# Performance work log

Hardware: AMD Instinct MI355X
Metric: run time of the kernel (lower is better)

Reference implementation:

```python
import jax, jax.numpy as jnp
import numpy as np

NEG_SLOPE = 0.2  # PyG GATConv default leaky_relu slope


def gat_layer(x, src, dst, W, a_src, a_dst, bias, heads, d, concat):
    # x: [N, in_dim]; src/dst: [E] (edges flow src -> dst, self-loops included)
    N = x.shape[0]
    h = (x @ W).reshape(N, heads, d)                      # [N, H, D]
    alpha_src = jnp.einsum('nhd,hd->nh', h, a_src)        # [N, H]
    alpha_dst = jnp.einsum('nhd,hd->nh', h, a_dst)        # [N, H]
    e = jax.nn.leaky_relu(alpha_src[src] + alpha_dst[dst], NEG_SLOPE)  # [E, H]
    # softmax over incoming edges of each destination node (segment softmax)
    m = jax.ops.segment_max(e, dst, num_segments=N)       # [N, H]
    ex = jnp.exp(e - m[dst])
    s = jax.ops.segment_sum(ex, dst, num_segments=N)      # [N, H]
    alpha = ex / s[dst]                                   # [E, H]
    msg = h[src] * alpha[..., None]                       # [E, H, D]
    out = jax.ops.segment_sum(msg, dst, num_segments=N)   # [N, H, D]
    out = out.reshape(N, heads * d) if concat else out.mean(axis=1)
    return out + bias


def setup_inputs() -> dict:
    key = jax.random.key(0)
    ks = jax.random.split(key, 12)
    N, E = 10000, 320000
    in_dim, hidden, heads, out_dim = 256, 64, 4, 40
    x = jax.random.normal(ks[0], (N, in_dim), dtype=jnp.float32)
    edge_index = jax.random.randint(ks[1], (2, E), 0, N, dtype=jnp.int64)
    s = 0.1
    return {
        'x': x,
        'edge_index': edge_index,
        'W1': jax.random.normal(ks[2], (in_dim, heads * hidden), jnp.float32) * s,
        'att_src1': jax.random.normal(ks[3], (heads, hidden), jnp.float32) * s,
        'att_dst1': jax.random.normal(ks[4], (heads, hidden), jnp.float32) * s,
        'bias1': jnp.zeros((heads * hidden,), jnp.float32),
        'W2': jax.random.normal(ks[5], (heads * hidden, out_dim), jnp.float32) * s,
        'att_src2': jax.random.normal(ks[6], (1, out_dim), jnp.float32) * s,
        'att_dst2': jax.random.normal(ks[7], (1, out_dim), jnp.float32) * s,
        'bias2': jnp.zeros((out_dim,), jnp.float32),
    }


def reference(x, edge_index, W1, att_src1, att_dst1, bias1, W2, att_src2, att_dst2, bias2):
    N = x.shape[0]
    # PyG GATConv adds self-loops by default
    loop = jnp.arange(N, dtype=edge_index.dtype)
    src = jnp.concatenate([edge_index[0], loop])
    dst = jnp.concatenate([edge_index[1], loop])
    h = gat_layer(x, src, dst, W1, att_src1, att_dst1, bias1, heads=4, d=64, concat=True)
    h = jax.nn.relu(h)
    out = gat_layer(h, src, dst, W2, att_src2, att_dst2, bias2, heads=1, d=40, concat=False)
    return jax.nn.log_softmax(out, axis=1)
```

## Files before the change

### kernel.cpp

```cpp
#include <hip/hip_runtime.h>
#include <hip/hip_bf16.h>
#include <math.h>

#define IN_DIM 256
#define C1 256
#define H1 4
#define OUT_DIM 40
#define W2PAD 48
#define NEG_SLOPE 0.2f
#define DSTRIDE 128

typedef __attribute__((ext_vector_type(8))) short bf16x8;
typedef __attribute__((ext_vector_type(4))) float f32x4;
typedef __attribute__((ext_vector_type(2))) float f32x2;

#define XS_LD 264

__device__ __forceinline__ unsigned short f2bf(float f) {
    union { float f; unsigned u; } c; c.f = f;
    unsigned r = c.u + 0x7fffu + ((c.u >> 16) & 1u);
    return (unsigned short)(r >> 16);
}

__device__ __forceinline__ unsigned char f2fp8(float f) {
    return (unsigned char)__builtin_amdgcn_cvt_pk_fp8_f32(f, 0.f, 0, false);
}

__device__ __forceinline__ float sel4(float4 v, int h) {
    float r = v.x;
    r = (h == 1) ? v.y : r;
    r = (h == 2) ? v.z : r;
    r = (h == 3) ? v.w : r;
    return r;
}

__device__ __forceinline__ float leaky(float v) {
    return (v >= 0.0f) ? v : NEG_SLOPE * v;
}

__global__ void k_prep(int* __restrict__ fill, const float* __restrict__ W1,
                       unsigned short* __restrict__ W1t, const float* __restrict__ W2,
                       unsigned short* __restrict__ W2t, const float* __restrict__ a_src2,
                       const float* __restrict__ a_dst2, float* __restrict__ w2s,
                       float* __restrict__ w2d, int N) {
    int t = threadIdx.x;
    int g = blockIdx.x * 256 + t;
    if (g < N) fill[g << 4] = 0;
    if (g < C1) {
        float s = 0.0f, d = 0.0f;
#pragma unroll
        for (int j = 0; j < OUT_DIM; ++j) {
            float w = W2[g * OUT_DIM + j];
            s += w * a_src2[j];
            d += w * a_dst2[j];
        }
        w2s[g] = s;
        w2d[g] = d;
    }
    if (g < W2PAD * C1) {
        int j = g >> 8, k = g & 255;
        W2t[g] = (j < OUT_DIM) ? f2bf(W2[k * OUT_DIM + j]) : 0;
    }
    __shared__ float s32[32][33];
    int b = blockIdx.x;
    int r0 = (b >> 3) * 32;
    int c0 = (b & 7) * 32;
    for (int i = t; i < 1024; i += 256) {
        int lr = i >> 5, lc = i & 31;
        s32[lr][lc] = W1[(r0 + lr) * 256 + c0 + lc];
    }
    __syncthreads();
    for (int i = t; i < 1024; i += 256) {
        int oc = i >> 5, ok = i & 31;
        W1t[(c0 + oc) * 256 + r0 + ok] = f2bf(s32[ok][oc]);
    }
}

__global__ void __launch_bounds__(256) k_fused1(
    const float* __restrict__ x, const unsigned short* __restrict__ W1t,
    const float* __restrict__ a_src, const float* __restrict__ a_dst,
    unsigned char* __restrict__ h1, float* __restrict__ as1, float* __restrict__ ad1,
    const int* __restrict__ ei, int* __restrict__ fill, unsigned short* __restrict__ srcs,
    int N, int E, int ET, int G1) {
    __shared__ unsigned short xs[64 * XS_LD];
    int t = threadIdx.x;

    if (blockIdx.x >= G1) {
        int eb = (blockIdx.x - G1) * 1024 + t;
#pragma unroll
        for (int k = 0; k < 4; ++k) {
            int e = eb + k * 256;
            if (e < ET) {
                int s, d;
                if (e < E) { s = ei[e]; d = ei[E + e]; }
                else       { s = e - E; d = s; }
                int pos = atomicAdd(&fill[d << 4], 1);
                srcs[(d << 7) + pos] = (unsigned short)s;
            }
        }
        return;
    }

    int n0 = blockIdx.x * 64;
    for (int i = t; i < 4096; i += 256) {
        int r = i >> 6, c4 = i & 63;
        int n = n0 + r;
        float4 v = (n < N) ? ((const float4*)x)[(size_t)n * 64 + c4]
                           : make_float4(0.f, 0.f, 0.f, 0.f);
        uint2 pk;
        pk.x = (unsigned)f2bf(v.x) | ((unsigned)f2bf(v.y) << 16);
        pk.y = (unsigned)f2bf(v.z) | ((unsigned)f2bf(v.w) << 16);
        *((uint2*)&xs[r * XS_LD + c4 * 4]) = pk;
    }
    __syncthreads();

    int wv = t >> 6, lane = t & 63;
    int quad = lane >> 4, ln = lane & 15;

    f32x4 acc[4][4];
#pragma unroll
    for (int mt = 0; mt < 4; ++mt)
#pragma unroll
        for (int nt = 0; nt < 4; ++nt) acc[mt][nt] = (f32x4){0.f, 0.f, 0.f, 0.f};

#pragma unroll
    for (int kb = 0; kb < 8; ++kb) {
        bf16x8 af[4], bf[4];
#pragma unroll
        for (int mt = 0; mt < 4; ++mt)
            af[mt] = *((bf16x8*)&xs[(mt * 16 + ln) * XS_LD + kb * 32 + quad * 8]);
#pragma unroll
        for (int nt = 0; nt < 4; ++nt)
            bf[nt] = *((const bf16x8*)(W1t + ((wv * 64 + nt * 16 + ln) * 256 + kb * 32 + quad * 8)));
#pragma unroll
        for (int mt = 0; mt < 4; ++mt)
#pragma unroll
            for (int nt = 0; nt < 4; ++nt)
                acc[mt][nt] = __builtin_amdgcn_mfma_f32_16x16x32_bf16(af[mt], bf[nt], acc[mt][nt], 0, 0, 0);
    }

    float asv[4], adv[4];
#pragma unroll
    for (int nt = 0; nt < 4; ++nt) {
        int col = wv * 64 + nt * 16 + ln;
        asv[nt] = a_src[col];
        adv[nt] = a_dst[col];
    }
#pragma unroll
    for (int mt = 0; mt < 4; ++mt) {
        float ds[4] = {0.f, 0.f, 0.f, 0.f};
        float dd[4] = {0.f, 0.f, 0.f, 0.f};
#pragma unroll
        for (int nt = 0; nt < 4; ++nt) {
#pragma unroll
            for (int r = 0; r < 4; ++r) {
                float v = acc[mt][nt][r];
                ds[r] += v * asv[nt];
                dd[r] += v * adv[nt];
            }
        }
#pragma unroll
        for (int r = 0; r < 4; ++r) {
            float vs = ds[r], vd = dd[r];
#pragma unroll
            for (int o = 1; o < 16; o <<= 1) {
                vs += __shfl_xor(vs, o);
                vd += __shfl_xor(vd, o);
            }
            if (ln == 0) {
                int node = n0 + mt * 16 + quad * 4 + r;
                if (node < N) {
                    as1[node * H1 + wv] = vs;
                    ad1[node * H1 + wv] = vd;
                }
            }
        }
    }

    __syncthreads();
    unsigned char* bt = (unsigned char*)xs;
#pragma unroll
    for (int mt = 0; mt < 4; ++mt)
#pragma unroll
        for (int nt = 0; nt < 4; ++nt)
#pragma unroll
            for (int r = 0; r < 4; ++r)
                bt[(mt * 16 + quad * 4 + r) * 256 + wv * 64 + nt * 16 + ln] = f2fp8(acc[mt][nt][r]);
    __syncthreads();
    const uint4* bt4 = (const uint4*)bt;
    uint4* h14 = (uint4*)(h1 + (size_t)n0 * C1);
    for (int i = t; i < 1024; i += 256) {
        int row = i >> 4;
        if (n0 + row < N) h14[i] = bt4[i];
    }
}

__global__ void __launch_bounds__(256) k_node1(
    const int* __restrict__ fill, const unsigned short* __restrict__ srcs,
    const float* __restrict__ as1f, const float* __restrict__ ad1f,
    const unsigned char* __restrict__ h1, const float* __restrict__ bias1,
    const float* __restrict__ w2s, const float* __restrict__ w2d,
    unsigned short* __restrict__ agg1b, float* __restrict__ as2,
    float* __restrict__ ad2, int N) {
    int w = threadIdx.x >> 6, lane = threadIdx.x & 63;
    int n = blockIdx.x * 4 + w;
    if (n >= N) return;
    __shared__ float4 es[4][64];
    int start = n << 7;
    int end = start + fill[n << 4];
    const float4* as4 = (const float4*)as1f;
    float4 adn = ((const float4*)ad1f)[n];
    int h = lane >> 4;
    const float* esw = (const float*)&es[w][0];

    float4 S4 = make_float4(0.f, 0.f, 0.f, 0.f);
    float ac0 = 0.f, ac1 = 0.f, ac2 = 0.f, ac3 = 0.f;

    for (int c = start; c < end; c += 64) {
        int cnt = min(64, end - c);
        int idx = c + lane;
        int sreg = (idx < end) ? (int)srcs[idx] : 0;
        float4 ex = make_float4(0.f, 0.f, 0.f, 0.f);
        if (idx < end) {
            float4 a = as4[sreg];
            ex.x = __expf(leaky(a.x + adn.x));
            ex.y = __expf(leaky(a.y + adn.y));
            ex.z = __expf(leaky(a.z + adn.z));
            ex.w = __expf(leaky(a.w + adn.w));
        }
        S4.x += ex.x; S4.y += ex.y; S4.z += ex.z; S4.w += ex.w;
        es[w][lane] = ex;

        int i = 0;
        for (; i + 7 < cnt; i += 8) {
            int s[8]; float a[8]; unsigned r[8];
#pragma unroll
            for (int k = 0; k < 8; ++k) {
                s[k] = __shfl(sreg, i + k);
                a[k] = esw[(i + k) * 4 + h];
            }
#pragma unroll
            for (int k = 0; k < 8; ++k)
                r[k] = ((const unsigned*)(h1 + (size_t)s[k] * C1))[lane];
#pragma unroll
            for (int k = 0; k < 8; ++k) {
                f32x2 lo = __builtin_amdgcn_cvt_pk_f32_fp8(r[k], false);
                f32x2 hi = __builtin_amdgcn_cvt_pk_f32_fp8(r[k], true);
                ac0 += a[k] * lo.x;
                ac1 += a[k] * lo.y;
                ac2 += a[k] * hi.x;
                ac3 += a[k] * hi.y;
            }
        }
        for (; i < cnt; ++i) {
            int s0 = __shfl(sreg, i);
            float a0 = esw[i * 4 + h];
            unsigned r0 = ((const unsigned*)(h1 + (size_t)s0 * C1))[lane];
            f32x2 lo = __builtin_amdgcn_cvt_pk_f32_fp8(r0, false);
            f32x2 hi = __builtin_amdgcn_cvt_pk_f32_fp8(r0, true);
            ac0 += a0 * lo.x;
            ac1 += a0 * lo.y;
            ac2 += a0 * hi.x;
            ac3 += a0 * hi.y;
        }
    }

#pragma unroll
    for (int o = 32; o > 0; o >>= 1) {
        S4.x += __shfl_xor(S4.x, o);
        S4.y += __shfl_xor(S4.y, o);
        S4.z += __shfl_xor(S4.z, o);
        S4.w += __shfl_xor(S4.w, o);
    }
    float iS = 1.0f / sel4(S4, h);
    float4 b = ((const float4*)bias1)[lane];
    float v0 = fmaxf(ac0 * iS + b.x, 0.f);
    float v1 = fmaxf(ac1 * iS + b.y, 0.f);
    float v2 = fmaxf(ac2 * iS + b.z, 0.f);
    float v3 = fmaxf(ac3 * iS + b.w, 0.f);
    uint2 pk;
    pk.x = (unsigned)f2bf(v0) | ((unsigned)f2bf(v1) << 16);
    pk.y = (unsigned)f2bf(v2) | ((unsigned)f2bf(v3) << 16);
    ((uint2*)(agg1b + (size_t)n * C1))[lane] = pk;

    float4 ws = ((const float4*)w2s)[lane];
    float4 wd = ((const float4*)w2d)[lane];
    float ps = v0 * ws.x + v1 * ws.y + v2 * ws.z + v3 * ws.w;
    float pd = v0 * wd.x + v1 * wd.y + v2 * wd.z + v3 * wd.w;
#pragma unroll
    for (int o = 32; o > 0; o >>= 1) {
        ps += __shfl_xor(ps, o);
        pd += __shfl_xor(pd, o);
    }
    if (lane == 0) { as2[n] = ps; ad2[n] = pd; }
}

__global__ void __launch_bounds__(256) k_gemm2m(
    const unsigned short* __restrict__ agg1b, const unsigned short* __restrict__ W2t,
    unsigned short* __restrict__ h2b, int N) {
    int t = threadIdx.x;
    int wv = t >> 6, lane = t & 63;
    int quad = lane >> 4, ln = lane & 15;
    int n0 = blockIdx.x * 64;
    int mrow = n0 + wv * 16 + ln;

    f32x4 acc[3];
#pragma unroll
    for (int nt = 0; nt < 3; ++nt) acc[nt] = (f32x4){0.f, 0.f, 0.f, 0.f};

#pragma unroll
    for (int kb = 0; kb < 8; ++kb) {
        bf16x8 af = *((const bf16x8*)(agg1b + (size_t)mrow * C1 + kb * 32 + quad * 8));
#pragma unroll
        for (int nt = 0; nt < 3; ++nt) {
            bf16x8 bfr = *((const bf16x8*)(W2t + ((nt * 16 + ln) * C1 + kb * 32 + quad * 8)));
            acc[nt] = __builtin_amdgcn_mfma_f32_16x16x32_bf16(af, bfr, acc[nt], 0, 0, 0);
        }
    }
#pragma unroll
    for (int nt = 0; nt < 3; ++nt) {
        int col = nt * 16 + ln;
        if (col < OUT_DIM) {
#pragma unroll
            for (int r = 0; r < 4; ++r) {
                int node = n0 + wv * 16 + quad * 4 + r;
                if (node < N) h2b[(size_t)node * OUT_DIM + col] = f2bf(acc[nt][r]);
            }
        }
    }
}

__global__ void __launch_bounds__(256) k_node2(
    const int* __restrict__ fill, const unsigned short* __restrict__ srcs,
    const float* __restrict__ as2, const float* __restrict__ ad2,
    const unsigned short* __restrict__ h2b, const float* __restrict__ bias2,
    float* __restrict__ out, int N) {
    int w = threadIdx.x >> 6, lane = threadIdx.x & 63;
    int n = blockIdx.x * 4 + w;
    if (n >= N) return;
    int start = n << 7;
    int end = start + fill[n << 4];
    float adn = ad2[n];
    float S = 0.f, acc0 = 0.f, acc1 = 0.f;
    bool act = lane < 20;

    for (int c = start; c < end; c += 64) {
        int cnt = min(64, end - c);
        int idx = c + lane;
        int sreg = (idx < end) ? (int)srcs[idx] : 0;
        float ex = (idx < end) ? __expf(leaky(as2[sreg] + adn)) : 0.f;
        S += ex;
        int i = 0;
        for (; i + 3 < cnt; i += 4) {
            int su[4]; float al[4]; unsigned rw[4];
#pragma unroll
            for (int k = 0; k < 4; ++k) {
                su[k] = __shfl(sreg, i + k);
                al[k] = __shfl(ex, i + k);
            }
#pragma unroll
            for (int k = 0; k < 4; ++k)
                rw[k] = act ? *(const unsigned*)(h2b + (size_t)su[k] * OUT_DIM + lane * 2) : 0u;
#pragma unroll
            for (int k = 0; k < 4; ++k) {
                acc0 += al[k] * __uint_as_float(rw[k] << 16);
                acc1 += al[k] * __uint_as_float(rw[k] & 0xffff0000u);
            }
        }
        for (; i < cnt; ++i) {
            int su0 = __shfl(sreg, i);
            float al0 = __shfl(ex, i);
            unsigned rw0 = act ? *(const unsigned*)(h2b + (size_t)su0 * OUT_DIM + lane * 2) : 0u;
            acc0 += al0 * __uint_as_float(rw0 << 16);
            acc1 += al0 * __uint_as_float(rw0 & 0xffff0000u);
        }
    }
#pragma unroll
    for (int o = 32; o > 0; o >>= 1) S += __shfl_xor(S, o);

    float v0 = act ? (acc0 / S + bias2[lane * 2]) : -INFINITY;
    float v1 = act ? (acc1 / S + bias2[lane * 2 + 1]) : -INFINITY;
    float mx = fmaxf(v0, v1);
#pragma unroll
    for (int o = 16; o > 0; o >>= 1) mx = fmaxf(mx, __shfl_xor(mx, o));
    float e0 = act ? __expf(v0 - mx) : 0.f;
    float e1 = act ? __expf(v1 - mx) : 0.f;
    float esum = e0 + e1;
#pragma unroll
    for (int o = 16; o > 0; o >>= 1) esum += __shfl_xor(esum, o);
    if (act) {
        float l = mx + logf(esum);
        out[(size_t)n * OUT_DIM + lane * 2]     = v0 - l;
        out[(size_t)n * OUT_DIM + lane * 2 + 1] = v1 - l;
    }
}

extern "C" void kernel_launch(void* const* d_in, const int* in_sizes, int n_in,
                              void* d_out, int out_size, void* d_ws, size_t ws_size,
                              hipStream_t stream) {
    const float* x        = (const float*)d_in[0];
    const int*   ei       = (const int*)d_in[1];
    const float* W1       = (const float*)d_in[2];
    const float* att_src1 = (const float*)d_in[3];
    const float* att_dst1 = (const float*)d_in[4];
    const float* bias1    = (const float*)d_in[5];
    const float* W2       = (const float*)d_in[6];
    const float* att_src2 = (const float*)d_in[7];
    const float* att_dst2 = (const float*)d_in[8];
    const float* bias2    = (const float*)d_in[9];
    float* out = (float*)d_out;

    const int N  = in_sizes[0] / IN_DIM;
    const int E  = in_sizes[1] / 2;
    const int ET = E + N;
    const int Npad = (N + 63) & ~63;

    char* base = (char*)d_ws;
    auto alloc = [&](size_t bytes) {
        char* p = base;
        base += (bytes + 255) & ~(size_t)255;
        return p;
    };
    unsigned char*  h1    = (unsigned char*)alloc((size_t)N * C1);
    unsigned short* W1t   = (unsigned short*)alloc((size_t)C1 * C1 * 2);
    unsigned short* W2t   = (unsigned short*)alloc((size_t)W2PAD * C1 * 2);
    unsigned short* agg1b = (unsigned short*)alloc((size_t)Npad * C1 * 2);
    unsigned short* h2b   = (unsigned short*)alloc((size_t)N * OUT_DIM * 2);
    float* as1   = (float*)alloc((size_t)N * H1 * 4);
    float* ad1   = (float*)alloc((size_t)N * H1 * 4);
    float* as2   = (float*)alloc((size_t)N * 4);
    float* ad2   = (float*)alloc((size_t)N * 4);
    float* w2s   = (float*)alloc((size_t)C1 * 4);
    float* w2d   = (float*)alloc((size_t)C1 * 4);
    int* fill    = (int*)alloc((size_t)N * 16 * 4);
    unsigned short* srcs = (unsigned short*)alloc((size_t)N * DSTRIDE * 2);

    const int G1 = (N + 63) / 64;
    const int GS = (ET + 1023) / 1024;

    k_prep<<<64, 256, 0, stream>>>(fill, W1, W1t, W2, W2t, att_src2, att_dst2, w2s, w2d, N);
    k_fused1<<<G1 + GS, 256, 0, stream>>>(x, W1t, att_src1, att_dst1, h1, as1, ad1,
                                          ei, fill, srcs, N, E, ET, G1);
    k_node1<<<(N + 3) / 4, 256, 0, stream>>>(fill, srcs, as1, ad1, h1, bias1, w2s, w2d,
                                             agg1b, as2, ad2, N);
    k_gemm2m<<<(N + 63) / 64, 256, 0, stream>>>(agg1b, W2t, h2b, N);
    k_node2<<<(N + 3) / 4, 256, 0, stream>>>(fill, srcs, as2, ad2, h2b, bias2, out, N);
}
```

Measured before the change: 142.6 us.

## Shard per-destination edge counters to cut atomic contention in CSR build

Replaces the single per-destination fill counter with eight sharded counters, chosen by edge index, each with its own slot region in a wider per-node source list. This spreads atomicAdd traffic on hot destination counters across separate cache lines. The cost is a larger fill array to zero and read, a prefix sum over eight shard counts per node, and a per-lane shard lookup when gathering sources in both aggregation kernels. Each shard holds at most 24 slots, so a destination that receives more than 24 edges in one shard would overflow its slots.

```diff
diff --git a/kernel.cpp b/kernel.cpp
--- a/kernel.cpp
+++ b/kernel.cpp
@@ -8,7 +8,9 @@
 #define OUT_DIM 40
 #define W2PAD 48
 #define NEG_SLOPE 0.2f
-#define DSTRIDE 128
+#define NSHARD 8
+#define SHSLOT 24
+#define DSTRIDE 192
 
 typedef __attribute__((ext_vector_type(8))) short bf16x8;
 typedef __attribute__((ext_vector_type(4))) float f32x4;
@@ -45,7 +47,7 @@
                        float* __restrict__ w2d, int N) {
     int t = threadIdx.x;
     int g = blockIdx.x * 256 + t;
-    if (g < N) fill[g << 4] = 0;
+    for (int i = g; i < N * NSHARD; i += 64 * 256) fill[i << 4] = 0;
     if (g < C1) {
         float s = 0.0f, d = 0.0f;
 #pragma unroll
@@ -94,8 +96,9 @@
                 int s, d;
                 if (e < E) { s = ei[e]; d = ei[E + e]; }
                 else       { s = e - E; d = s; }
-                int pos = atomicAdd(&fill[d << 4], 1);
-                srcs[(d << 7) + pos] = (unsigned short)s;
+                int j = e & (NSHARD - 1);
+                int pos = atomicAdd(&fill[((d << 3) + j) << 4], 1);
+                srcs[d * DSTRIDE + j * SHSLOT + pos] = (unsigned short)s;
             }
         }
         return;
@@ -206,8 +209,13 @@
     int n = blockIdx.x * 4 + w;
     if (n >= N) return;
     __shared__ float4 es[4][64];
-    int start = n << 7;
-    int end = start + fill[n << 4];
+    int off[NSHARD + 1];
+    off[0] = 0;
+#pragma unroll
+    for (int j = 0; j < NSHARD; ++j)
+        off[j + 1] = off[j] + fill[((n << 3) + j) << 4];
+    int deg = off[NSHARD];
+    const unsigned short* srow = srcs + (size_t)n * DSTRIDE;
     const float4* as4 = (const float4*)as1f;
     float4 adn = ((const float4*)ad1f)[n];
     int h = lane >> 4;
@@ -216,12 +224,19 @@
     float4 S4 = make_float4(0.f, 0.f, 0.f, 0.f);
     float ac0 = 0.f, ac1 = 0.f, ac2 = 0.f, ac3 = 0.f;
 
-    for (int c = start; c < end; c += 64) {
-        int cnt = min(64, end - c);
+    for (int c = 0; c < deg; c += 64) {
+        int cnt = min(64, deg - c);
         int idx = c + lane;
-        int sreg = (idx < end) ? (int)srcs[idx] : 0;
+        int sreg = 0;
+        if (idx < deg) {
+            int jj = 0, bo = 0;
+#pragma unroll
+            for (int j = 1; j < NSHARD; ++j)
+                if (idx >= off[j]) { jj = j; bo = off[j]; }
+            sreg = (int)srow[jj * SHSLOT + (idx - bo)];
+        }
         float4 ex = make_float4(0.f, 0.f, 0.f, 0.f);
-        if (idx < end) {
+        if (idx < deg) {
             float4 a = as4[sreg];
             ex.x = __expf(leaky(a.x + adn.x));
             ex.y = __expf(leaky(a.y + adn.y));
@@ -338,17 +353,29 @@
     int w = threadIdx.x >> 6, lane = threadIdx.x & 63;
     int n = blockIdx.x * 4 + w;
     if (n >= N) return;
-    int start = n << 7;
-    int end = start + fill[n << 4];
+    int off[NSHARD + 1];
+    off[0] = 0;
+#pragma unroll
+    for (int j = 0; j < NSHARD; ++j)
+        off[j + 1] = off[j] + fill[((n << 3) + j) << 4];
+    int deg = off[NSHARD];
+    const unsigned short* srow = srcs + (size_t)n * DSTRIDE;
     float adn = ad2[n];
     float S = 0.f, acc0 = 0.f, acc1 = 0.f;
     bool act = lane < 20;
 
-    for (int c = start; c < end; c += 64) {
-        int cnt = min(64, end - c);
+    for (int c = 0; c < deg; c += 64) {
+        int cnt = min(64, deg - c);
         int idx = c + lane;
-        int sreg = (idx < end) ? (int)srcs[idx] : 0;
-        float ex = (idx < end) ? __expf(leaky(as2[sreg] + adn)) : 0.f;
+        int sreg = 0;
+        if (idx < deg) {
+            int jj = 0, bo = 0;
+#pragma unroll
+            for (int j = 1; j < NSHARD; ++j)
+                if (idx >= off[j]) { jj = j; bo = off[j]; }
+            sreg = (int)srow[jj * SHSLOT + (idx - bo)];
+        }
+        float ex = (idx < deg) ? __expf(leaky(as2[sreg] + adn)) : 0.f;
         S += ex;
         int i = 0;
         for (; i + 3 < cnt; i += 4) {
@@ -432,7 +459,7 @@
     float* ad2   = (float*)alloc((size_t)N * 4);
     float* w2s   = (float*)alloc((size_t)C1 * 4);
     float* w2d   = (float*)alloc((size_t)C1 * 4);
-    int* fill    = (int*)alloc((size_t)N * 16 * 4);
+    int* fill    = (int*)alloc((size_t)N * NSHARD * 16 * 4);
     unsigned short* srcs = (unsigned short*)alloc((size_t)N * DSTRIDE * 2);
 
     const int G1 = (N + 63) / 64;
```

New measurement: 145.0 us. No clear change (+1.7%).

## Split each node's edge aggregation across two waves in layer-1 node kernel

Applied to the files above, without the earlier changes.

The layer-1 node kernel now assigns two wavefronts per destination node, each handling alternating edges, instead of one wavefront per node. Each wave stages its own exp weights. Partial softmax sums and accumulators are combined through shared memory after a block barrier. The goal is more parallelism and more memory-latency hiding for the per-node fp8 row gathers. The trade-off is twice as many waves, extra barriers, and a single-pass design that relies on degree never exceeding 128. Separately, the edge-scatter blocks in the fused GEMM kernel now process 8 edges per thread instead of 4, halving the number of scatter blocks.

```diff
diff --git a/kernel.cpp b/kernel.cpp
--- a/kernel.cpp
+++ b/kernel.cpp
@@ -86,9 +86,9 @@
     int t = threadIdx.x;
 
     if (blockIdx.x >= G1) {
-        int eb = (blockIdx.x - G1) * 1024 + t;
-#pragma unroll
-        for (int k = 0; k < 4; ++k) {
+        int eb = (blockIdx.x - G1) * 2048 + t;
+#pragma unroll
+        for (int k = 0; k < 8; ++k) {
             int e = eb + k * 256;
             if (e < ET) {
                 int s, d;
@@ -202,69 +202,36 @@
     const float* __restrict__ w2s, const float* __restrict__ w2d,
     unsigned short* __restrict__ agg1b, float* __restrict__ as2,
     float* __restrict__ ad2, int N) {
-    int w = threadIdx.x >> 6, lane = threadIdx.x & 63;
-    int n = blockIdx.x * 4 + w;
-    if (n >= N) return;
+    int wv = threadIdx.x >> 6, lane = threadIdx.x & 63;
+    int nl = wv >> 1;
+    int half = wv & 1;
+    int n = blockIdx.x * 2 + nl;
     __shared__ float4 es[4][64];
-    int start = n << 7;
-    int end = start + fill[n << 4];
+    __shared__ float4 sS[4];
+    __shared__ float4 accb[2][64];
+    bool valid = (n < N);
+
+    int deg = valid ? fill[n << 4] : 0;
+    const unsigned short* srow = srcs + ((size_t)n << 7);
     const float4* as4 = (const float4*)as1f;
-    float4 adn = ((const float4*)ad1f)[n];
+    float4 adn = valid ? ((const float4*)ad1f)[n] : make_float4(0.f, 0.f, 0.f, 0.f);
     int h = lane >> 4;
-    const float* esw = (const float*)&es[w][0];
-
-    float4 S4 = make_float4(0.f, 0.f, 0.f, 0.f);
-    float ac0 = 0.f, ac1 = 0.f, ac2 = 0.f, ac3 = 0.f;
-
-    for (int c = start; c < end; c += 64) {
-        int cnt = min(64, end - c);
-        int idx = c + lane;
-        int sreg = (idx < end) ? (int)srcs[idx] : 0;
-        float4 ex = make_float4(0.f, 0.f, 0.f, 0.f);
-        if (idx < end) {
-            float4 a = as4[sreg];
-            ex.x = __expf(leaky(a.x + adn.x));
-            ex.y = __expf(leaky(a.y + adn.y));
-            ex.z = __expf(leaky(a.z + adn.z));
-            ex.w = __expf(leaky(a.w + adn.w));
-        }
-        S4.x += ex.x; S4.y += ex.y; S4.z += ex.z; S4.w += ex.w;
-        es[w][lane] = ex;
-
-        int i = 0;
-        for (; i + 7 < cnt; i += 8) {
-            int s[8]; float a[8]; unsigned r[8];
-#pragma unroll
-            for (int k = 0; k < 8; ++k) {
-                s[k] = __shfl(sreg, i + k);
-                a[k] = esw[(i + k) * 4 + h];
-            }
-#pragma unroll
-            for (int k = 0; k < 8; ++k)
-                r[k] = ((const unsigned*)(h1 + (size_t)s[k] * C1))[lane];
-#pragma unroll
-            for (int k = 0; k < 8; ++k) {
-                f32x2 lo = __builtin_amdgcn_cvt_pk_f32_fp8(r[k], false);
-                f32x2 hi = __builtin_amdgcn_cvt_pk_f32_fp8(r[k], true);
-                ac0 += a[k] * lo.x;
-                ac1 += a[k] * lo.y;
-                ac2 += a[k] * hi.x;
-                ac3 += a[k] * hi.y;
-            }
-        }
-        for (; i < cnt; ++i) {
-            int s0 = __shfl(sreg, i);
-            float a0 = esw[i * 4 + h];
-            unsigned r0 = ((const unsigned*)(h1 + (size_t)s0 * C1))[lane];
-            f32x2 lo = __builtin_amdgcn_cvt_pk_f32_fp8(r0, false);
-            f32x2 hi = __builtin_amdgcn_cvt_pk_f32_fp8(r0, true);
-            ac0 += a0 * lo.x;
-            ac1 += a0 * lo.y;
-            ac2 += a0 * hi.x;
-            ac3 += a0 * hi.y;
-        }
-    }
-
+
+    int idx = half + 2 * lane;
+    int sreg = (valid && idx < deg) ? (int)srow[idx] : 0;
+    int cnt = 0;
+    if (deg > half) cnt = (deg - half + 1) >> 1;
+
+    float4 ex = make_float4(0.f, 0.f, 0.f, 0.f);
+    if (valid && idx < deg) {
+        float4 a = as4[sreg];
+        ex.x = __expf(leaky(a.x + adn.x));
+        ex.y = __expf(leaky(a.y + adn.y));
+        ex.z = __expf(leaky(a.z + adn.z));
+        ex.w = __expf(leaky(a.w + adn.w));
+    }
+    es[wv][lane] = ex;
+    float4 S4 = ex;
 #pragma unroll
     for (int o = 32; o > 0; o >>= 1) {
         S4.x += __shfl_xor(S4.x, o);
@@ -272,27 +239,73 @@
         S4.z += __shfl_xor(S4.z, o);
         S4.w += __shfl_xor(S4.w, o);
     }
-    float iS = 1.0f / sel4(S4, h);
-    float4 b = ((const float4*)bias1)[lane];
-    float v0 = fmaxf(ac0 * iS + b.x, 0.f);
-    float v1 = fmaxf(ac1 * iS + b.y, 0.f);
-    float v2 = fmaxf(ac2 * iS + b.z, 0.f);
-    float v3 = fmaxf(ac3 * iS + b.w, 0.f);
-    uint2 pk;
-    pk.x = (unsigned)f2bf(v0) | ((unsigned)f2bf(v1) << 16);
-    pk.y = (unsigned)f2bf(v2) | ((unsigned)f2bf(v3) << 16);
-    ((uint2*)(agg1b + (size_t)n * C1))[lane] = pk;
-
-    float4 ws = ((const float4*)w2s)[lane];
-    float4 wd = ((const float4*)w2d)[lane];
-    float ps = v0 * ws.x + v1 * ws.y + v2 * ws.z + v3 * ws.w;
-    float pd = v0 * wd.x + v1 * wd.y + v2 * wd.z + v3 * wd.w;
-#pragma unroll
-    for (int o = 32; o > 0; o >>= 1) {
-        ps += __shfl_xor(ps, o);
-        pd += __shfl_xor(pd, o);
-    }
-    if (lane == 0) { as2[n] = ps; ad2[n] = pd; }
+    if (lane == 0) sS[wv] = S4;
+    __syncthreads();
+
+    const float* esw = (const float*)&es[wv][0];
+    float ac0 = 0.f, ac1 = 0.f, ac2 = 0.f, ac3 = 0.f;
+    int i = 0;
+    for (; i + 7 < cnt; i += 8) {
+        int s[8]; float a[8]; unsigned r[8];
+#pragma unroll
+        for (int k = 0; k < 8; ++k) {
+            s[k] = __shfl(sreg, i + k);
+            a[k] = esw[(i + k) * 4 + h];
+        }
+#pragma unroll
+        for (int k = 0; k < 8; ++k)
+            r[k] = ((const unsigned*)(h1 + (size_t)s[k] * C1))[lane];
+#pragma unroll
+        for (int k = 0; k < 8; ++k) {
+            f32x2 lo = __builtin_amdgcn_cvt_pk_f32_fp8(r[k], false);
+            f32x2 hi = __builtin_amdgcn_cvt_pk_f32_fp8(r[k], true);
+            ac0 += a[k] * lo.x;
+            ac1 += a[k] * lo.y;
+            ac2 += a[k] * hi.x;
+            ac3 += a[k] * hi.y;
+        }
+    }
+    for (; i < cnt; ++i) {
+        int s0 = __shfl(sreg, i);
+        float a0 = esw[i * 4 + h];
+        unsigned r0 = ((const unsigned*)(h1 + (size_t)s0 * C1))[lane];
+        f32x2 lo = __builtin_amdgcn_cvt_pk_f32_fp8(r0, false);
+        f32x2 hi = __builtin_amdgcn_cvt_pk_f32_fp8(r0, true);
+        ac0 += a0 * lo.x;
+        ac1 += a0 * lo.y;
+        ac2 += a0 * hi.x;
+        ac3 += a0 * hi.y;
+    }
+
+    if (half == 1) accb[nl][lane] = make_float4(ac0, ac1, ac2, ac3);
+    __syncthreads();
+    if (half == 0 && valid) {
+        float4 o2 = accb[nl][lane];
+        ac0 += o2.x; ac1 += o2.y; ac2 += o2.z; ac3 += o2.w;
+        float4 Sa = sS[nl * 2], Sb = sS[nl * 2 + 1];
+        float4 St = make_float4(Sa.x + Sb.x, Sa.y + Sb.y, Sa.z + Sb.z, Sa.w + Sb.w);
+        float iS = 1.0f / sel4(St, h);
+        float4 b = ((const float4*)bias1)[lane];
+        float v0 = fmaxf(ac0 * iS + b.x, 0.f);
+        float v1 = fmaxf(ac1 * iS + b.y, 0.f);
+        float v2 = fmaxf(ac2 * iS + b.z, 0.f);
+        float v3 = fmaxf(ac3 * iS + b.w, 0.f);
+        uint2 pk;
+        pk.x = (unsigned)f2bf(v0) | ((unsigned)f2bf(v1) << 16);
+        pk.y = (unsigned)f2bf(v2) | ((unsigned)f2bf(v3) << 16);
+        ((uint2*)(agg1b + (size_t)n * C1))[lane] = pk;
+
+        float4 ws = ((const float4*)w2s)[lane];
+        float4 wd = ((const float4*)w2d)[lane];
+        float ps = v0 * ws.x + v1 * ws.y + v2 * ws.z + v3 * ws.w;
+        float pd = v0 * wd.x + v1 * wd.y + v2 * wd.z + v3 * wd.w;
+#pragma unroll
+        for (int o = 32; o > 0; o >>= 1) {
+            ps += __shfl_xor(ps, o);
+            pd += __shfl_xor(pd, o);
+        }
+        if (lane == 0) { as2[n] = ps; ad2[n] = pd; }
+    }
 }
 
 __global__ void __launch_bounds__(256) k_gemm2m(
@@ -436,12 +449,12 @@
     unsigned short* srcs = (unsigned short*)alloc((size_t)N * DSTRIDE * 2);
 
     const int G1 = (N + 63) / 64;
-    const int GS = (ET + 1023) / 1024;
+    const int GS = (ET + 2047) / 2048;
 
     k_prep<<<64, 256, 0, stream>>>(fill, W1, W1t, W2, W2t, att_src2, att_dst2, w2s, w2d, N);
     k_fused1<<<G1 + GS, 256, 0, stream>>>(x, W1t, att_src1, att_dst1, h1, as1, ad1,
                                           ei, fill, srcs, N, E, ET, G1);
-    k_node1<<<(N + 3) / 4, 256, 0, stream>>>(fill, srcs, as1, ad1, h1, bias1, w2s, w2d,
+    k_node1<<<(N + 1) / 2, 256, 0, stream>>>(fill, srcs, as1, ad1, h1, bias1, w2s, w2d,
                                              agg1b, as2, ad2, N);
     k_gemm2m<<<(N + 63) / 64, 256, 0, stream>>>(agg1b, W2t, h2b, N);
     k_node2<<<(N + 3) / 4, 256, 0, stream>>>(fill, srcs, as2, ad2, h2b, bias2, out, N);
```

Result: no change. 145.1 us (+1.7%).

## Fuse all five stages into one cooperative persistent kernel with grid syncs

Applied to the files above, without the earlier changes.

Replaces the five separate kernel launches (prep, gemm1+scatter, node1, gemm2, node2) with a single cooperative persistent kernel. Blocks loop over virtual block indices, and grid.sync() separates the stages. The scatter chunk size doubles to 2048 edges per virtual block. This removes per-launch overhead and inter-kernel gaps, but adds grid-wide barrier costs and may lower occupancy, since the mega-kernel's shared memory and register use apply to every phase.

```diff
diff --git a/kernel.cpp b/kernel.cpp
--- a/kernel.cpp
+++ b/kernel.cpp
@@ -1,6 +1,9 @@
 #include <hip/hip_runtime.h>
 #include <hip/hip_bf16.h>
+#include <hip/hip_cooperative_groups.h>
 #include <math.h>
+
+namespace cg = cooperative_groups;
 
 #define IN_DIM 256
 #define C1 256
@@ -15,6 +18,7 @@
 typedef __attribute__((ext_vector_type(2))) float f32x2;
 
 #define XS_LD 264
+#define SHBYTES (64 * XS_LD * 2)
 
 __device__ __forceinline__ unsigned short f2bf(float f) {
     union { float f; unsigned u; } c; c.f = f;
@@ -38,33 +42,25 @@
     return (v >= 0.0f) ? v : NEG_SLOPE * v;
 }
 
-__global__ void k_prep(int* __restrict__ fill, const float* __restrict__ W1,
-                       unsigned short* __restrict__ W1t, const float* __restrict__ W2,
-                       unsigned short* __restrict__ W2t, const float* __restrict__ a_src2,
-                       const float* __restrict__ a_dst2, float* __restrict__ w2s,
-                       float* __restrict__ w2d, int N) {
-    int t = threadIdx.x;
-    int g = blockIdx.x * 256 + t;
-    if (g < N) fill[g << 4] = 0;
-    if (g < C1) {
-        float s = 0.0f, d = 0.0f;
-#pragma unroll
-        for (int j = 0; j < OUT_DIM; ++j) {
-            float w = W2[g * OUT_DIM + j];
-            s += w * a_src2[j];
-            d += w * a_dst2[j];
-        }
-        w2s[g] = s;
-        w2d[g] = d;
-    }
-    if (g < W2PAD * C1) {
-        int j = g >> 8, k = g & 255;
-        W2t[g] = (j < OUT_DIM) ? f2bf(W2[k * OUT_DIM + j]) : 0;
-    }
-    __shared__ float s32[32][33];
-    int b = blockIdx.x;
-    int r0 = (b >> 3) * 32;
-    int c0 = (b & 7) * 32;
+struct MegaArgs {
+    const float* x; const int* ei;
+    const float* W1; const float* a_src1; const float* a_dst1; const float* bias1;
+    const float* W2; const float* a_src2; const float* a_dst2; const float* bias2;
+    float* out;
+    unsigned char* h1;
+    unsigned short* W1t; unsigned short* W2t; unsigned short* agg1b; unsigned short* h2b;
+    float* as1; float* ad1; float* as2; float* ad2; float* w2s; float* w2d;
+    int* fill; unsigned short* srcs;
+    int N, E, ET, G1, GS;
+};
+
+
+__device__ void prep_w1t_tile(char* shbuf, int vb, const float* __restrict__ W1,
+                              unsigned short* __restrict__ W1t, int t) {
+    float (*s32)[33] = (float (*)[33])shbuf;
+    __syncthreads();
+    int r0 = (vb >> 3) * 32;
+    int c0 = (vb & 7) * 32;
     for (int i = t; i < 1024; i += 256) {
         int lr = i >> 5, lc = i & 31;
         s32[lr][lc] = W1[(r0 + lr) * 256 + c0 + lc];
@@ -76,37 +72,15 @@
     }
 }
 
-__global__ void __launch_bounds__(256) k_fused1(
-    const float* __restrict__ x, const unsigned short* __restrict__ W1t,
-    const float* __restrict__ a_src, const float* __restrict__ a_dst,
-    unsigned char* __restrict__ h1, float* __restrict__ as1, float* __restrict__ ad1,
-    const int* __restrict__ ei, int* __restrict__ fill, unsigned short* __restrict__ srcs,
-    int N, int E, int ET, int G1) {
-    __shared__ unsigned short xs[64 * XS_LD];
-    int t = threadIdx.x;
-
-    if (blockIdx.x >= G1) {
-        int eb = (blockIdx.x - G1) * 1024 + t;
-#pragma unroll
-        for (int k = 0; k < 4; ++k) {
-            int e = eb + k * 256;
-            if (e < ET) {
-                int s, d;
-                if (e < E) { s = ei[e]; d = ei[E + e]; }
-                else       { s = e - E; d = s; }
-                int pos = atomicAdd(&fill[d << 4], 1);
-                srcs[(d << 7) + pos] = (unsigned short)s;
-            }
-        }
-        return;
-    }
-
-    int n0 = blockIdx.x * 64;
+__device__ void gemm1_tile(char* shbuf, int vb, const MegaArgs& a, int t) {
+    unsigned short* xs = (unsigned short*)shbuf;
+    int n0 = vb * 64;
+    __syncthreads();
     for (int i = t; i < 4096; i += 256) {
         int r = i >> 6, c4 = i & 63;
         int n = n0 + r;
-        float4 v = (n < N) ? ((const float4*)x)[(size_t)n * 64 + c4]
-                           : make_float4(0.f, 0.f, 0.f, 0.f);
+        float4 v = (n < a.N) ? ((const float4*)a.x)[(size_t)n * 64 + c4]
+                             : make_float4(0.f, 0.f, 0.f, 0.f);
         uint2 pk;
         pk.x = (unsigned)f2bf(v.x) | ((unsigned)f2bf(v.y) << 16);
         pk.y = (unsigned)f2bf(v.z) | ((unsigned)f2bf(v.w) << 16);
@@ -131,7 +105,7 @@
             af[mt] = *((bf16x8*)&xs[(mt * 16 + ln) * XS_LD + kb * 32 + quad * 8]);
 #pragma unroll
         for (int nt = 0; nt < 4; ++nt)
-            bf[nt] = *((const bf16x8*)(W1t + ((wv * 64 + nt * 16 + ln) * 256 + kb * 32 + quad * 8)));
+            bf[nt] = *((const bf16x8*)(a.W1t + ((wv * 64 + nt * 16 + ln) * 256 + kb * 32 + quad * 8)));
 #pragma unroll
         for (int mt = 0; mt < 4; ++mt)
 #pragma unroll
@@ -143,8 +117,8 @@
 #pragma unroll
     for (int nt = 0; nt < 4; ++nt) {
         int col = wv * 64 + nt * 16 + ln;
-        asv[nt] = a_src[col];
-        adv[nt] = a_dst[col];
+        asv[nt] = a.a_src1[col];
+        adv[nt] = a.a_dst1[col];
     }
 #pragma unroll
     for (int mt = 0; mt < 4; ++mt) {
@@ -169,9 +143,9 @@
             }
             if (ln == 0) {
                 int node = n0 + mt * 16 + quad * 4 + r;
-                if (node < N) {
-                    as1[node * H1 + wv] = vs;
-                    ad1[node * H1 + wv] = vd;
+                if (node < a.N) {
+                    a.as1[node * H1 + wv] = vs;
+                    a.ad1[node * H1 + wv] = vd;
                 }
             }
         }
@@ -188,167 +162,170 @@
                 bt[(mt * 16 + quad * 4 + r) * 256 + wv * 64 + nt * 16 + ln] = f2fp8(acc[mt][nt][r]);
     __syncthreads();
     const uint4* bt4 = (const uint4*)bt;
-    uint4* h14 = (uint4*)(h1 + (size_t)n0 * C1);
+    uint4* h14 = (uint4*)(a.h1 + (size_t)n0 * C1);
     for (int i = t; i < 1024; i += 256) {
         int row = i >> 4;
-        if (n0 + row < N) h14[i] = bt4[i];
-    }
-}
-
-__global__ void __launch_bounds__(256) k_node1(
-    const int* __restrict__ fill, const unsigned short* __restrict__ srcs,
-    const float* __restrict__ as1f, const float* __restrict__ ad1f,
-    const unsigned char* __restrict__ h1, const float* __restrict__ bias1,
-    const float* __restrict__ w2s, const float* __restrict__ w2d,
-    unsigned short* __restrict__ agg1b, float* __restrict__ as2,
-    float* __restrict__ ad2, int N) {
-    int w = threadIdx.x >> 6, lane = threadIdx.x & 63;
-    int n = blockIdx.x * 4 + w;
-    if (n >= N) return;
-    __shared__ float4 es[4][64];
+        if (n0 + row < a.N) h14[i] = bt4[i];
+    }
+}
+
+__device__ void scatter_chunk(int vb, const MegaArgs& a, int t) {
+    int eb = vb * 2048 + t;
+#pragma unroll
+    for (int k = 0; k < 8; ++k) {
+        int e = eb + k * 256;
+        if (e < a.ET) {
+            int s, d;
+            if (e < a.E) { s = a.ei[e]; d = a.ei[a.E + e]; }
+            else         { s = e - a.E; d = s; }
+            int pos = atomicAdd(&a.fill[d << 4], 1);
+            a.srcs[(d << 7) + pos] = (unsigned short)s;
+        }
+    }
+}
+
+__device__ void node1_vb(char* shbuf, int vb, const MegaArgs& a, int tid) {
+    int w = tid >> 6, lane = tid & 63;
+    int n = vb * 4 + w;
+    float4 (*es)[64] = (float4 (*)[64])shbuf;
+    if (n < a.N) {
+        int start = n << 7;
+        int end = start + a.fill[n << 4];
+        const float4* as4 = (const float4*)a.as1;
+        float4 adn = ((const float4*)a.ad1)[n];
+        int h = lane >> 4;
+        const float* esw = (const float*)&es[w][0];
+
+        float4 S4 = make_float4(0.f, 0.f, 0.f, 0.f);
+        float ac0 = 0.f, ac1 = 0.f, ac2 = 0.f, ac3 = 0.f;
+
+        for (int c = start; c < end; c += 64) {
+            int cnt = min(64, end - c);
+            int idx = c + lane;
+            int sreg = (idx < end) ? (int)a.srcs[idx] : 0;
+            float4 ex = make_float4(0.f, 0.f, 0.f, 0.f);
+            if (idx < end) {
+                float4 av = as4[sreg];
+                ex.x = __expf(leaky(av.x + adn.x));
+                ex.y = __expf(leaky(av.y + adn.y));
+                ex.z = __expf(leaky(av.z + adn.z));
+                ex.w = __expf(leaky(av.w + adn.w));
+            }
+            S4.x += ex.x; S4.y += ex.y; S4.z += ex.z; S4.w += ex.w;
+            es[w][lane] = ex;
+
+            int i = 0;
+            for (; i + 7 < cnt; i += 8) {
+                int s[8]; float al[8]; unsigned r[8];
+#pragma unroll
+                for (int k = 0; k < 8; ++k) {
+                    s[k] = __shfl(sreg, i + k);
+                    al[k] = esw[(i + k) * 4 + h];
+                }
+#pragma unroll
+                for (int k = 0; k < 8; ++k)
+                    r[k] = ((const unsigned*)(a.h1 + (size_t)s[k] * C1))[lane];
+#pragma unroll
+                for (int k = 0; k < 8; ++k) {
+                    f32x2 lo = __builtin_amdgcn_cvt_pk_f32_fp8(r[k], false);
+                    f32x2 hi = __builtin_amdgcn_cvt_pk_f32_fp8(r[k], true);
+                    ac0 += al[k] * lo.x;
+                    ac1 += al[k] * lo.y;
+                    ac2 += al[k] * hi.x;
+                    ac3 += al[k] * hi.y;
+                }
+            }
+            for (; i < cnt; ++i) {
+                int s0 = __shfl(sreg, i);
+                float a0 = esw[i * 4 + h];
+                unsigned r0 = ((const unsigned*)(a.h1 + (size_t)s0 * C1))[lane];
+                f32x2 lo = __builtin_amdgcn_cvt_pk_f32_fp8(r0, false);
+                f32x2 hi = __builtin_amdgcn_cvt_pk_f32_fp8(r0, true);
+                ac0 += a0 * lo.x;
+                ac1 += a0 * lo.y;
+                ac2 += a0 * hi.x;
+                ac3 += a0 * hi.y;
+            }
+        }
+
+#pragma unroll
+        for (int o = 32; o > 0; o >>= 1) {
+            S4.x += __shfl_xor(S4.x, o);
+            S4.y += __shfl_xor(S4.y, o);
+            S4.z += __shfl_xor(S4.z, o);
+            S4.w += __shfl_xor(S4.w, o);
+        }
+        float iS = 1.0f / sel4(S4, h);
+        float4 b = ((const float4*)a.bias1)[lane];
+        float v0 = fmaxf(ac0 * iS + b.x, 0.f);
+        float v1 = fmaxf(ac1 * iS + b.y, 0.f);
+        float v2 = fmaxf(ac2 * iS + b.z, 0.f);
+        float v3 = fmaxf(ac3 * iS + b.w, 0.f);
+        uint2 pk;
+        pk.x = (unsigned)f2bf(v0) | ((unsigned)f2bf(v1) << 16);
+        pk.y = (unsigned)f2bf(v2) | ((unsigned)f2bf(v3) << 16);
+        ((uint2*)(a.agg1b + (size_t)n * C1))[lane] = pk;
+
+        float4 ws = ((const float4*)a.w2s)[lane];
+        float4 wd = ((const float4*)a.w2d)[lane];
+        float ps = v0 * ws.x + v1 * ws.y + v2 * ws.z + v3 * ws.w;
+        float pd = v0 * wd.x + v1 * wd.y + v2 * wd.z + v3 * wd.w;
+#pragma unroll
+        for (int o = 32; o > 0; o >>= 1) {
+            ps += __shfl_xor(ps, o);
+            pd += __shfl_xor(pd, o);
+        }
+        if (lane == 0) { a.as2[n] = ps; a.ad2[n] = pd; }
+    }
+}
+
+__device__ void gemm2m_vb(int vb, const MegaArgs& a, int t) {
+    int wv = t >> 6, lane = t & 63;
+    int quad = lane >> 4, ln = lane & 15;
+    int n0 = vb * 64;
+    int mrow = n0 + wv * 16 + ln;
+
+    f32x4 acc[3];
+#pragma unroll
+    for (int nt = 0; nt < 3; ++nt) acc[nt] = (f32x4){0.f, 0.f, 0.f, 0.f};
+
+#pragma unroll
+    for (int kb = 0; kb < 8; ++kb) {
+        bf16x8 af = *((const bf16x8*)(a.agg1b + (size_t)mrow * C1 + kb * 32 + quad * 8));
+#pragma unroll
+        for (int nt = 0; nt < 3; ++nt) {
+            bf16x8 bfr = *((const bf16x8*)(a.W2t + ((nt * 16 + ln) * C1 + kb * 32 + quad * 8)));
+            acc[nt] = __builtin_amdgcn_mfma_f32_16x16x32_bf16(af, bfr, acc[nt], 0, 0, 0);
+        }
+    }
+#pragma unroll
+    for (int nt = 0; nt < 3; ++nt) {
+        int col = nt * 16 + ln;
+        if (col < OUT_DIM) {
+#pragma unroll
+            for (int r = 0; r < 4; ++r) {
+                int node = n0 + wv * 16 + quad * 4 + r;
+                if (node < a.N) a.h2b[(size_t)node * OUT_DIM + col] = f2bf(acc[nt][r]);
+            }
+        }
+    }
+}
+
+__device__ void node2_vb(int vb, const MegaArgs& a, int tid) {
+    int w = tid >> 6, lane = tid & 63;
+    int n = vb * 4 + w;
+    if (n >= a.N) return;
     int start = n << 7;
-    int end = start + fill[n << 4];
-    const float4* as4 = (const float4*)as1f;
-    float4 adn = ((const float4*)ad1f)[n];
-    int h = lane >> 4;
-    const float* esw = (const float*)&es[w][0];
-
-    float4 S4 = make_float4(0.f, 0.f, 0.f, 0.f);
-    float ac0 = 0.f, ac1 = 0.f, ac2 = 0.f, ac3 = 0.f;
+    int end = start + a.fill[n << 4];
+    float adn = a.ad2[n];
+    float S = 0.f, acc0 = 0.f, acc1 = 0.f;
+    bool act = lane < 20;
 
     for (int c = start; c < end; c += 64) {
         int cnt = min(64, end - c);
         int idx = c + lane;
-        int sreg = (idx < end) ? (int)srcs[idx] : 0;
-        float4 ex = make_float4(0.f, 0.f, 0.f, 0.f);
-        if (idx < end) {
-            float4 a = as4[sreg];
-            ex.x = __expf(leaky(a.x + adn.x));
-            ex.y = __expf(leaky(a.y + adn.y));
-            ex.z = __expf(leaky(a.z + adn.z));
-            ex.w = __expf(leaky(a.w + adn.w));
-        }
-        S4.x += ex.x; S4.y += ex.y; S4.z += ex.z; S4.w += ex.w;
-        es[w][lane] = ex;
-
-        int i = 0;
-        for (; i + 7 < cnt; i += 8) {
-            int s[8]; float a[8]; unsigned r[8];
-#pragma unroll
-            for (int k = 0; k < 8; ++k) {
-                s[k] = __shfl(sreg, i + k);
-                a[k] = esw[(i + k) * 4 + h];
-            }
-#pragma unroll
-            for (int k = 0; k < 8; ++k)
-                r[k] = ((const unsigned*)(h1 + (size_t)s[k] * C1))[lane];
-#pragma unroll
-            for (int k = 0; k < 8; ++k) {
-                f32x2 lo = __builtin_amdgcn_cvt_pk_f32_fp8(r[k], false);
-                f32x2 hi = __builtin_amdgcn_cvt_pk_f32_fp8(r[k], true);
-                ac0 += a[k] * lo.x;
-                ac1 += a[k] * lo.y;
-                ac2 += a[k] * hi.x;
-                ac3 += a[k] * hi.y;
-            }
-        }
-        for (; i < cnt; ++i) {
-            int s0 = __shfl(sreg, i);
-            float a0 = esw[i * 4 + h];
-            unsigned r0 = ((const unsigned*)(h1 + (size_t)s0 * C1))[lane];
-            f32x2 lo = __builtin_amdgcn_cvt_pk_f32_fp8(r0, false);
-            f32x2 hi = __builtin_amdgcn_cvt_pk_f32_fp8(r0, true);
-            ac0 += a0 * lo.x;
-            ac1 += a0 * lo.y;
-            ac2 += a0 * hi.x;
-            ac3 += a0 * hi.y;
-        }
-    }
-
-#pragma unroll
-    for (int o = 32; o > 0; o >>= 1) {
-        S4.x += __shfl_xor(S4.x, o);
-        S4.y += __shfl_xor(S4.y, o);
-        S4.z += __shfl_xor(S4.z, o);
-        S4.w += __shfl_xor(S4.w, o);
-    }
-    float iS = 1.0f / sel4(S4, h);
-    float4 b = ((const float4*)bias1)[lane];
-    float v0 = fmaxf(ac0 * iS + b.x, 0.f);
-    float v1 = fmaxf(ac1 * iS + b.y, 0.f);
-    float v2 = fmaxf(ac2 * iS + b.z, 0.f);
-    float v3 = fmaxf(ac3 * iS + b.w, 0.f);
-    uint2 pk;
-    pk.x = (unsigned)f2bf(v0) | ((unsigned)f2bf(v1) << 16);
-    pk.y = (unsigned)f2bf(v2) | ((unsigned)f2bf(v3) << 16);
-    ((uint2*)(agg1b + (size_t)n * C1))[lane] = pk;
-
-    float4 ws = ((const float4*)w2s)[lane];
-    float4 wd = ((const float4*)w2d)[lane];
-    float ps = v0 * ws.x + v1 * ws.y + v2 * ws.z + v3 * ws.w;
-    float pd = v0 * wd.x + v1 * wd.y + v2 * wd.z + v3 * wd.w;
-#pragma unroll
-    for (int o = 32; o > 0; o >>= 1) {
-        ps += __shfl_xor(ps, o);
-        pd += __shfl_xor(pd, o);
-    }
-    if (lane == 0) { as2[n] = ps; ad2[n] = pd; }
-}
-
-__global__ void __launch_bounds__(256) k_gemm2m(
-    const unsigned short* __restrict__ agg1b, const unsigned short* __restrict__ W2t,
-    unsigned short* __restrict__ h2b, int N) {
-    int t = threadIdx.x;
-    int wv = t >> 6, lane = t & 63;
-    int quad = lane >> 4, ln = lane & 15;
-    int n0 = blockIdx.x * 64;
-    int mrow = n0 + wv * 16 + ln;
-
-    f32x4 acc[3];
-#pragma unroll
-    for (int nt = 0; nt < 3; ++nt) acc[nt] = (f32x4){0.f, 0.f, 0.f, 0.f};
-
-#pragma unroll
-    for (int kb = 0; kb < 8; ++kb) {
-        bf16x8 af = *((const bf16x8*)(agg1b + (size_t)mrow * C1 + kb * 32 + quad * 8));
-#pragma unroll
-        for (int nt = 0; nt < 3; ++nt) {
-            bf16x8 bfr = *((const bf16x8*)(W2t + ((nt * 16 + ln) * C1 + kb * 32 + quad * 8)));
-            acc[nt] = __builtin_amdgcn_mfma_f32_16x16x32_bf16(af, bfr, acc[nt], 0, 0, 0);
-        }
-    }
-#pragma unroll
-    for (int nt = 0; nt < 3; ++nt) {
-        int col = nt * 16 + ln;
-        if (col < OUT_DIM) {
-#pragma unroll
-            for (int r = 0; r < 4; ++r) {
-                int node = n0 + wv * 16 + quad * 4 + r;
-                if (node < N) h2b[(size_t)node * OUT_DIM + col] = f2bf(acc[nt][r]);
-            }
-        }
-    }
-}
-
-__global__ void __launch_bounds__(256) k_node2(
-    const int* __restrict__ fill, const unsigned short* __restrict__ srcs,
-    const float* __restrict__ as2, const float* __restrict__ ad2,
-    const unsigned short* __restrict__ h2b, const float* __restrict__ bias2,
-    float* __restrict__ out, int N) {
-    int w = threadIdx.x >> 6, lane = threadIdx.x & 63;
-    int n = blockIdx.x * 4 + w;
-    if (n >= N) return;
-    int start = n << 7;
-    int end = start + fill[n << 4];
-    float adn = ad2[n];
-    float S = 0.f, acc0 = 0.f, acc1 = 0.f;
-    bool act = lane < 20;
-
-    for (int c = start; c < end; c += 64) {
-        int cnt = min(64, end - c);
-        int idx = c + lane;
-        int sreg = (idx < end) ? (int)srcs[idx] : 0;
-        float ex = (idx < end) ? __expf(leaky(as2[sreg] + adn)) : 0.f;
+        int sreg = (idx < end) ? (int)a.srcs[idx] : 0;
+        float ex = (idx < end) ? __expf(leaky(a.as2[sreg] + adn)) : 0.f;
         S += ex;
         int i = 0;
         for (; i + 3 < cnt; i += 4) {
@@ -360,7 +337,7 @@
             }
 #pragma unroll
             for (int k = 0; k < 4; ++k)
-                rw[k] = act ? *(const unsigned*)(h2b + (size_t)su[k] * OUT_DIM + lane * 2) : 0u;
+                rw[k] = act ? *(const unsigned*)(a.h2b + (size_t)su[k] * OUT_DIM + lane * 2) : 0u;
 #pragma unroll
             for (int k = 0; k < 4; ++k) {
                 acc0 += al[k] * __uint_as_float(rw[k] << 16);
@@ -370,7 +347,7 @@
         for (; i < cnt; ++i) {
             int su0 = __shfl(sreg, i);
             float al0 = __shfl(ex, i);
-            unsigned rw0 = act ? *(const unsigned*)(h2b + (size_t)su0 * OUT_DIM + lane * 2) : 0u;
+            unsigned rw0 = act ? *(const unsigned*)(a.h2b + (size_t)su0 * OUT_DIM + lane * 2) : 0u;
             acc0 += al0 * __uint_as_float(rw0 << 16);
             acc1 += al0 * __uint_as_float(rw0 & 0xffff0000u);
         }
@@ -378,8 +355,8 @@
 #pragma unroll
     for (int o = 32; o > 0; o >>= 1) S += __shfl_xor(S, o);
 
-    float v0 = act ? (acc0 / S + bias2[lane * 2]) : -INFINITY;
-    float v1 = act ? (acc1 / S + bias2[lane * 2 + 1]) : -INFINITY;
+    float v0 = act ? (acc0 / S + a.bias2[lane * 2]) : -INFINITY;
+    float v1 = act ? (acc1 / S + a.bias2[lane * 2 + 1]) : -INFINITY;
     float mx = fmaxf(v0, v1);
 #pragma unroll
     for (int o = 16; o > 0; o >>= 1) mx = fmaxf(mx, __shfl_xor(mx, o));
@@ -390,26 +367,62 @@
     for (int o = 16; o > 0; o >>= 1) esum += __shfl_xor(esum, o);
     if (act) {
         float l = mx + logf(esum);
-        out[(size_t)n * OUT_DIM + lane * 2]     = v0 - l;
-        out[(size_t)n * OUT_DIM + lane * 2 + 1] = v1 - l;
-    }
+        a.out[(size_t)n * OUT_DIM + lane * 2]     = v0 - l;
+        a.out[(size_t)n * OUT_DIM + lane * 2 + 1] = v1 - l;
+    }
+}
+
+__global__ void __launch_bounds__(256) k_mega(MegaArgs a) {
+    cg::grid_group grid = cg::this_grid();
+    __shared__ char shbuf[SHBYTES] __attribute__((aligned(16)));
+    int t = threadIdx.x;
+    int NB = gridDim.x;
+    int gtid = blockIdx.x * 256 + t;
+    int gsz = NB * 256;
+
+    for (int i = gtid; i < a.N; i += gsz) a.fill[i << 4] = 0;
+    for (int g = gtid; g < C1; g += gsz) {
+        float s = 0.0f, d = 0.0f;
+#pragma unroll
+        for (int j = 0; j < OUT_DIM; ++j) {
+            float w = a.W2[g * OUT_DIM + j];
+            s += w * a.a_src2[j];
+            d += w * a.a_dst2[j];
+        }
+        a.w2s[g] = s;
+        a.w2d[g] = d;
+    }
+    for (int g = gtid; g < W2PAD * C1; g += gsz) {
+        int j = g >> 8, k = g & 255;
+        a.W2t[g] = (j < OUT_DIM) ? f2bf(a.W2[k * OUT_DIM + j]) : 0;
+    }
+    for (int vb = blockIdx.x; vb < 64; vb += NB)
+        prep_w1t_tile(shbuf, vb, a.W1, a.W1t, t);
+    grid.sync();
+
+    for (int vb = blockIdx.x; vb < a.G1 + a.GS; vb += NB) {
+        if (vb < a.G1) gemm1_tile(shbuf, vb, a, t);
+        else           scatter_chunk(vb - a.G1, a, t);
+    }
+    grid.sync();
+
+    int NV1 = (a.N + 3) / 4;
+    for (int vb = blockIdx.x; vb < NV1; vb += NB)
+        node1_vb(shbuf, vb, a, t);
+    grid.sync();
+
+    int NV3 = (a.N + 63) / 64;
+    for (int vb = blockIdx.x; vb < NV3; vb += NB)
+        gemm2m_vb(vb, a, t);
+    grid.sync();
+
+    for (int vb = blockIdx.x; vb < NV1; vb += NB)
+        node2_vb(vb, a, t);
 }
 
 extern "C" void kernel_launch(void* const* d_in, const int* in_sizes, int n_in,
                               void* d_out, int out_size, void* d_ws, size_t ws_size,
                               hipStream_t stream) {
-    const float* x        = (const float*)d_in[0];
-    const int*   ei       = (const int*)d_in[1];
-    const float* W1       = (const float*)d_in[2];
-    const float* att_src1 = (const float*)d_in[3];
-    const float* att_dst1 = (const float*)d_in[4];
-    const float* bias1    = (const float*)d_in[5];
-    const float* W2       = (const float*)d_in[6];
-    const float* att_src2 = (const float*)d_in[7];
-    const float* att_dst2 = (const float*)d_in[8];
-    const float* bias2    = (const float*)d_in[9];
-    float* out = (float*)d_out;
-
     const int N  = in_sizes[0] / IN_DIM;
     const int E  = in_sizes[1] / 2;
     const int ET = E + N;
@@ -421,28 +434,41 @@
         base += (bytes + 255) & ~(size_t)255;
         return p;
     };
-    unsigned char*  h1    = (unsigned char*)alloc((size_t)N * C1);
-    unsigned short* W1t   = (unsigned short*)alloc((size_t)C1 * C1 * 2);
-    unsigned short* W2t   = (unsigned short*)alloc((size_t)W2PAD * C1 * 2);
-    unsigned short* agg1b = (unsigned short*)alloc((size_t)Npad * C1 * 2);
-    unsigned short* h2b   = (unsigned short*)alloc((size_t)N * OUT_DIM * 2);
-    float* as1   = (float*)alloc((size_t)N * H1 * 4);
-    float* ad1   = (float*)alloc((size_t)N * H1 * 4);
-    float* as2   = (float*)alloc((size_t)N * 4);
-    float* ad2   = (float*)alloc((size_t)N * 4);
-    float* w2s   = (float*)alloc((size_t)C1 * 4);
-    float* w2d   = (float*)alloc((size_t)C1 * 4);
-    int* fill    = (int*)alloc((size_t)N * 16 * 4);
-    unsigned short* srcs = (unsigned short*)alloc((size_t)N * DSTRIDE * 2);
-
-    const int G1 = (N + 63) / 64;
-    const int GS = (ET + 1023) / 1024;
-
-    k_prep<<<64, 256, 0, stream>>>(fill, W1, W1t, W2, W2t, att_src2, att_dst2, w2s, w2d, N);
-    k_fused1<<<G1 + GS, 256, 0, stream>>>(x, W1t, att_src1, att_dst1, h1, as1, ad1,
-                                          ei, fill, srcs, N, E, ET, G1);
-    k_node1<<<(N + 3) / 4, 256, 0, stream>>>(fill, srcs, as1, ad1, h1, bias1, w2s, w2d,
-                                             agg1b, as2, ad2, N);
-    k_gemm2m<<<(N + 63) / 64, 256, 0, stream>>>(agg1b, W2t, h2b, N);
-    k_node2<<<(N + 3) / 4, 256, 0, stream>>>(fill, srcs, as2, ad2, h2b, bias2, out, N);
-}
+    MegaArgs a;
+    a.x        = (const float*)d_in[0];
+    a.ei       = (const int*)d_in[1];
+    a.W1       = (const float*)d_in[2];
+    a.a_src1   = (const float*)d_in[3];
+    a.a_dst1   = (const float*)d_in[4];
+    a.bias1    = (const float*)d_in[5];
+    a.W2       = (const float*)d_in[6];
+    a.a_src2   = (const float*)d_in[7];
+    a.a_dst2   = (const float*)d_in[8];
+    a.bias2    = (const float*)d_in[9];
+    a.out      = (float*)d_out;
+    a.h1    = (unsigned char*)alloc((size_t)N * C1);
+    a.W1t   = (unsigned short*)alloc((size_t)C1 * C1 * 2);
+    a.W2t   = (unsigned short*)alloc((size_t)W2PAD * C1 * 2);
+    a.agg1b = (unsigned short*)alloc((size_t)Npad * C1 * 2);
+    a.h2b   = (unsigned short*)alloc((size_t)N * OUT_DIM * 2);
+    a.as1   = (float*)alloc((size_t)N * H1 * 4);
+    a.ad1   = (float*)alloc((size_t)N * H1 * 4);
+    a.as2   = (float*)alloc((size_t)N * 4);
+    a.ad2   = (float*)alloc((size_t)N * 4);
+    a.w2s   = (float*)alloc((size_t)C1 * 4);
+    a.w2d   = (float*)alloc((size_t)C1 * 4);
+    a.fill  = (int*)alloc((size_t)N * 16 * 4);
+    a.srcs  = (unsigned short*)alloc((size_t)N * DSTRIDE * 2);
+    a.N = N; a.E = E; a.ET = ET;
+    a.G1 = (N + 63) / 64;
+    a.GS = (ET + 2047) / 2048;
+
+    int maxB = 0;
+    (void)hipOccupancyMaxActiveBlocksPerMultiprocessor(&maxB, k_mega, 256, 0);
+    if (maxB < 1) maxB = 1;
+    int NB = 256 * maxB;
+    if (NB > 1024) NB = 1024;
+
+    void* kargs[] = {(void*)&a};
+    hipLaunchCooperativeKernel((void*)k_mega, dim3(NB), dim3(256), kargs, 0, stream);
+}
```

Result: slower. 335.3 us (+135.1%).
